# Performance work log

Hardware: AMD Instinct MI355X
Metric: run time of the kernel (lower is better)

The kernel has to match this reference:

```python
import jax, jax.numpy as jnp
import numpy as np

MUL0, MUL1 = 128, 64            # scalar (0e) and vector (1o) multiplicities
B = 8192                        # batch of nodes
SQRT3 = 3.0 ** 0.5
SQRT6 = 6.0 ** 0.5

# path normalization (e3nn 'component' irrep norm / 'element' path norm):
# coeff_ins = sqrt(dim(ir_out) / fan_in(i_out)), fan_in = sum_{ins -> i_out} mul1*mul2
A_0E = (1.0 / (MUL0 * MUL0 + MUL1 * MUL1)) ** 0.5   # paths (0,0,0)+(1,1,0)
A_1O = (3.0 / (MUL0 * MUL1 + MUL1 * MUL0)) ** 0.5   # paths (0,1,1)+(1,0,1)
A_1E = (3.0 / (MUL1 * MUL1)) ** 0.5                  # path  (1,1,1)


def _levi_civita():
    eps = np.zeros((3, 3, 3), dtype=np.float32)
    eps[0, 1, 2] = eps[1, 2, 0] = eps[2, 0, 1] = 1.0
    eps[0, 2, 1] = eps[2, 1, 0] = eps[1, 0, 2] = -1.0
    return jnp.asarray(eps)


def setup_inputs() -> dict:
    key = jax.random.key(0)
    ks = jax.random.split(key, 7)
    return {
        "x1": jax.random.normal(ks[0], (B, MUL0 + 3 * MUL1), dtype=jnp.float32),
        "x2": jax.random.normal(ks[1], (B, MUL0 + 3 * MUL1), dtype=jnp.float32),
        "w000": jax.random.normal(ks[2], (MUL0, MUL0, MUL0), dtype=jnp.float32),
        "w011": jax.random.normal(ks[3], (MUL0, MUL1, MUL1), dtype=jnp.float32),
        "w101": jax.random.normal(ks[4], (MUL1, MUL0, MUL1), dtype=jnp.float32),
        "w110": jax.random.normal(ks[5], (MUL1, MUL1, MUL0), dtype=jnp.float32),
        "w111": jax.random.normal(ks[6], (MUL1, MUL1, MUL1), dtype=jnp.float32),
    }


def reference(x1, x2, w000, w011, w101, w110, w111):
    b = x1.shape[0]
    # split irreps: scalars [b, 128], vectors [b, 64, 3]
    s1, v1 = x1[:, :MUL0], x1[:, MUL0:].reshape(b, MUL1, 3)
    s2, v2 = x2[:, :MUL0], x2[:, MUL0:].reshape(b, MUL1, 3)

    # 0e output: 0e x 0e -> 0e (w3j = 1) and 1o x 1o -> 0e (w3j = delta/sqrt3)
    out0 = A_0E * (
        jnp.einsum("uvw,bu,bv->bw", w000, s1, s2)
        + jnp.einsum("uvw,bui,bvi->bw", w110, v1, v2) / SQRT3
    )

    # 1o output: 0e x 1o -> 1o and 1o x 0e -> 1o (w3j = delta/sqrt3)
    out1o = (A_1O / SQRT3) * (
        jnp.einsum("uvw,bu,bvi->bwi", w011, s1, v2)
        + jnp.einsum("uvw,bui,bv->bwi", w101, v1, s2)
    )

    # 1e output: 1o x 1o -> 1e (w3j = levi-civita / sqrt6)
    eps = _levi_civita()
    out1e = (A_1E / SQRT6) * jnp.einsum("uvw,bui,bvj,ijk->bwk", w111, v1, v2, eps)

    return jnp.concatenate(
        [out0, out1o.reshape(b, -1), out1e.reshape(b, -1)], axis=-1
    )  # [b, 128 + 192 + 192] = [b, 512]
```

## Files before the change

kernel.cpp:

```cpp
#include <hip/hip_runtime.h>
#include <stdint.h>


typedef _Float16 f16;
typedef f16 f16x8 __attribute__((ext_vector_type(8)));
typedef float f32x4 __attribute__((ext_vector_type(4)));
typedef int i32x4 __attribute__((ext_vector_type(4)));

#define OFF_W000 0u
#define OFF_W110 2097152u
#define OFF_W011 2621440u
#define OFF_W101 3145728u
#define OFF_W111 3670016u
#define OFF_XS1  3932160u
#define OFF_XS2  4980736u
#define OFF_XV1  6029312u
#define OFF_XV2  7602176u
#define OFF_S0A  9175040u
#define OFF_S0B  10223616u
#define OFF_S1O  13369344u
#define WS_ELEMS 14942208u

#define SC_0E 0.006987712429686843f
#define SC_1O 0.0078125f
#define SC_1E 0.011048543456039806f

__global__ void tile_all_k(const float* __restrict__ w000, const float* __restrict__ w011,
                           const float* __restrict__ w101, const float* __restrict__ w110,
                           const float* __restrict__ w111, const float* __restrict__ x1,
                           const float* __restrict__ x2, f16* __restrict__ ws)
{
  unsigned tid = blockIdx.x*256u + threadIdx.x;
  if (tid < 2097152u) {
    unsigned e=tid&7u, n=(tid>>3)&127u, q=(tid>>10)&3u, p=(tid>>12)&1u, u=(tid>>13)&127u, vh=(tid>>20)&1u;
    unsigned v = vh*64u + p*32u + q*8u + e;
    ws[OFF_W000+tid] = (f16)w000[u*16384u + v*128u + n];
    return;
  }
  tid -= 2097152u;
  if (tid < 524288u) {
    unsigned e=tid&7u, n=(tid>>3)&127u, q=(tid>>10)&3u, p=(tid>>12)&1u, u=tid>>13;
    unsigned v = p*32u + q*8u + e;
    ws[OFF_W110+tid] = (f16)(w110[u*8192u + v*128u + n] * 0.5773502691896258f);
    return;
  }
  tid -= 524288u;
  if (tid < 524288u) {
    unsigned e=tid&7u, n=(tid>>3)&63u, q=(tid>>9)&3u, p=(tid>>11)&1u, u=tid>>12;
    unsigned v = p*32u + q*8u + e;
    ws[OFF_W011+tid] = (f16)w011[u*4096u + v*64u + n];
    return;
  }
  tid -= 524288u;
  if (tid < 524288u) {
    unsigned e=tid&7u, n=(tid>>3)&63u, q=(tid>>9)&3u, p=(tid>>11)&1u, u=tid>>12;
    unsigned v = p*32u + q*8u + e;
    ws[OFF_W101+tid] = (f16)w101[v*8192u + u*64u + n];
    return;
  }
  tid -= 524288u;
  if (tid < 262144u) {
    unsigned e=tid&7u, n=(tid>>3)&63u, q=(tid>>9)&3u, p=(tid>>11)&1u, u=tid>>12;
    unsigned v = p*32u + q*8u + e;
    ws[OFF_W111+tid] = (f16)w111[u*4096u + v*64u + n];
    return;
  }
  tid -= 262144u;
  if (tid < 1048576u) {
    unsigned e=tid&7u, r=(tid>>3)&127u, uo=(tid>>10)&15u, rt=tid>>14;
    ws[OFF_XS1+tid] = (f16)x1[(rt*128u+r)*320u + uo*8u + e];
    return;
  }
  tid -= 1048576u;
  if (tid < 1572864u) {
    unsigned e=tid&7u, r=(tid>>3)&127u, ov=(tid>>10)&7u, rest=tid>>13;
    unsigned i=rest%3u, rt=rest/3u;
    ws[OFF_XV1+tid] = (f16)x1[(rt*128u+r)*320u + 128u + (ov*8u+e)*3u + i];
    return;
  }
  tid -= 1572864u;
  if (tid < 1048576u) {
    unsigned e=tid&7u, r=(tid>>3)&127u, uo=(tid>>10)&15u, rt=tid>>14;
    ws[OFF_XS2+tid] = (f16)x2[(rt*128u+r)*320u + uo*8u + e];
    return;
  }
  tid -= 1048576u;
  {
    unsigned e=tid&7u, r=(tid>>3)&127u, ov=(tid>>10)&7u, rest=tid>>13;
    unsigned i=rest%3u, rt=rest/3u;
    ws[OFF_XV2+tid] = (f16)x2[(rt*128u+r)*320u + 128u + (ov*8u+e)*3u + i];
  }
}

#define GLD16(g,l) __builtin_amdgcn_global_load_lds( \
    (const __attribute__((address_space(1))) unsigned int*)(g), \
    (__attribute__((address_space(3))) unsigned int*)(l), 16, 0, 0)

#define WAITV(n) asm volatile("s_waitcnt vmcnt(" #n ")" ::: "memory")

template<int N, bool NEG, int SS>
__device__ __forceinline__ void run_phase(const f16* __restrict__ Wt,
    const f16* __restrict__ aW, const f16* __restrict__ bW, int bRow, int h,
    f16* sW, f16* sAw, f32x4 (&acc)[4][4])
{
  constexpr int S     = N/64;
  constexpr int TILEB = N*64;
  constexpr int PAIRB = 2*TILEB;
  constexpr int TILEE = N*32;
  constexpr int PAIRE = 2*TILEE;
  constexpr int M     = SS*8;
  const int lane = threadIdx.x & 63, wid = threadIdx.x >> 6;
  const int q = lane >> 4, r15 = lane & 15;

  WAITV(0);

  f16x8 br[4][2];
#pragma unroll
  for (int mt=0; mt<4; ++mt)
#pragma unroll
    for (int o=0; o<2; ++o)
      br[mt][o] = *(const f16x8*)(bW + (o*4+q)*1024 + (bRow + mt*16 + r15)*8);
#pragma unroll
  for (int mt=0; mt<4; ++mt)
#pragma unroll
    for (int o=0; o<2; ++o) {
      i32x4 tmp = __builtin_bit_cast(i32x4, br[mt][o]);
      asm volatile("" :: "v"(tmp));
    }

  const int wchunk = wid*S*1024;
  auto stPair = [&](int p, int slot){
    const char* s = (const char*)Wt + (size_t)p*PAIRB + wchunk;
    char* d = (char*)sW + slot*PAIRB + wchunk;
#pragma unroll
    for (int tt=0; tt<2; ++tt)
#pragma unroll
      for (int c=0; c<S; ++c)
        GLD16(s + tt*TILEB + c*1024 + lane*16, d + tt*TILEB + c*1024);
  };
  auto stA = [&](int ss2){
    GLD16((const char*)(aW + ss2*1024) + lane*16, (char*)sAw + (ss2&1)*1024);
  };

  stA(0); stPair(0,0); stPair(1,1);

#pragma unroll 1
  for (int ss = 0; ss < SS; ++ss) {
    f16x8 aR[4];
#pragma unroll
    for (int k = 0; k < 8; ++k) {
      const int m = ss*8 + k;
      if (k == 7) {
        if (ss+1 < SS) { if constexpr (S==1) WAITV(3); else WAITV(5); }
        else           WAITV(0);
      } else {
        if constexpr (S==1) WAITV(2); else WAITV(4);
      }
      __builtin_amdgcn_s_barrier();
      __builtin_amdgcn_sched_barrier(0);
      if (k == 6 && ss+1 < SS) stA(ss+1);
      if (m+2 < M) stPair(m+2, (k+2)&3);
      if (k == 0) {
#pragma unroll
        for (int mt=0; mt<4; ++mt)
          aR[mt] = *(const f16x8*)(sAw + (ss&1)*512 + (mt*16+r15)*8);
      }
      f16x8 af[4][2];
#pragma unroll
      for (int mt=0; mt<4; ++mt) {
        f16 av = aR[mt][k];
        if constexpr (NEG) av = -av;
        af[mt][0] = av * br[mt][0];
        af[mt][1] = av * br[mt][1];
      }
#pragma unroll
      for (int tt=0; tt<2; ++tt) {
        const f16* W = sW + (k&3)*PAIRE + tt*TILEE;
#pragma unroll
        for (int nt=0; nt<4; ++nt) {
          f16x8 bw = *(const f16x8*)(W + (q*N + h*64 + nt*16 + r15)*8);
#pragma unroll
          for (int mt=0; mt<4; ++mt)
            acc[mt][nt] = __builtin_amdgcn_mfma_f32_16x16x32_f16(af[mt][tt], bw, acc[mt][nt], 0,0,0);
        }
      }
    }
  }
  __builtin_amdgcn_s_barrier();
  __builtin_amdgcn_sched_barrier(0);
}

__global__ __launch_bounds__(256, 2)
void tp_main(f16* __restrict__ ws, float* __restrict__ out)
{
  __shared__ f16 smem[36864];
  f16* sW = smem;
  const int lane = threadIdx.x & 63, wid = threadIdx.x >> 6;
  f16* sAw = smem + 32768 + wid*1024;
  const int q = lane >> 4, r15 = lane & 15;

  f32x4 acc[4][4];
#pragma unroll
  for (int a=0;a<4;++a)
#pragma unroll
    for (int b=0;b<4;++b) acc[a][b] = (f32x4){0.f,0.f,0.f,0.f};

  const int bid = blockIdx.x;

  if (bid < 128) {
    const int rt = bid >> 1, vh = bid & 1;
    const int rgrp = wid >> 1, h = wid & 1;
    const f16* aW = ws + OFF_XS1 + rt*16384 + rgrp*512;
    const f16* bW = ws + OFF_XS2 + rt*16384 + vh*8192;
    run_phase<128,false,16>(ws + OFF_W000 + vh*1048576u, aW, bW, rgrp*64, h, sW, sAw, acc);
    const int rowb = rt*128 + rgrp*64;
    if (vh == 0) {
#pragma unroll
      for (int mt=0;mt<4;++mt)
#pragma unroll
        for (int nt=0;nt<4;++nt)
#pragma unroll
          for (int rg=0;rg<4;++rg)
            out[(rowb+mt*16+q*4+rg)*512 + h*64+nt*16+r15] = SC_0E*acc[mt][nt][rg];
    } else {
      f16* slab = ws + OFF_S0A;
#pragma unroll
      for (int mt=0;mt<4;++mt)
#pragma unroll
        for (int nt=0;nt<4;++nt)
#pragma unroll
          for (int rg=0;rg<4;++rg)
            slab[(rowb+mt*16+q*4+rg)*128 + h*64+nt*16+r15] = (f16)(SC_0E*acc[mt][nt][rg]);
    }
  } else if (bid < 224) {
    const int id = bid-128, i = id%3, rt = id/3;
    const int rgrp = wid, ro = rgrp & 1, sub = rgrp >> 1;
    const int rtt = rt*2 + sub;
    const f16* aW = ws + OFF_XS1 + rtt*16384 + ro*512;
    const f16* bW = ws + OFF_XV2 + (rtt*3+i)*8192;
    run_phase<64,false,16>(ws + OFF_W011, aW, bW, ro*64, 0, sW, sAw, acc);
    const int rowb = rt*256 + rgrp*64;
#pragma unroll
    for (int mt=0;mt<4;++mt)
#pragma unroll
      for (int nt=0;nt<4;++nt)
#pragma unroll
        for (int rg=0;rg<4;++rg)
          out[(rowb+mt*16+q*4+rg)*512 + 128 + 3*(nt*16+r15) + i] = SC_1O*acc[mt][nt][rg];
  } else if (bid < 320) {
    const int id = bid-224, i = id%3, rt = id/3;
    const int rgrp = wid, ro = rgrp & 1, sub = rgrp >> 1;
    const int rtt = rt*2 + sub;
    const f16* aW = ws + OFF_XS2 + rtt*16384 + ro*512;
    const f16* bW = ws + OFF_XV1 + (rtt*3+i)*8192;
    run_phase<64,false,16>(ws + OFF_W101, aW, bW, ro*64, 0, sW, sAw, acc);
    const int rowb = rt*256 + rgrp*64;
    f16* slab = ws + OFF_S1O;
#pragma unroll
    for (int mt=0;mt<4;++mt)
#pragma unroll
      for (int nt=0;nt<4;++nt)
#pragma unroll
        for (int rg=0;rg<4;++rg)
          slab[(rowb+mt*16+q*4+rg)*192 + 3*(nt*16+r15) + i] = (f16)(SC_1O*acc[mt][nt][rg]);
  } else if (bid < 416) {
    const int id = bid-320, kk = id%3, rt = id/3;
    int i = kk+1; if (i>2) i-=3;
    int j = kk+2; if (j>2) j-=3;
    const int rgrp = wid, ro = rgrp & 1, sub = rgrp >> 1;
    const int rtt = rt*2 + sub;
    run_phase<64,false,8>(ws + OFF_W111,
        ws + OFF_XV1 + (rtt*3+i)*8192 + ro*512, ws + OFF_XV2 + (rtt*3+j)*8192,
        ro*64, 0, sW, sAw, acc);
    run_phase<64,true,8>(ws + OFF_W111,
        ws + OFF_XV1 + (rtt*3+j)*8192 + ro*512, ws + OFF_XV2 + (rtt*3+i)*8192,
        ro*64, 0, sW, sAw, acc);
    const int rowb = rt*256 + rgrp*64;
#pragma unroll
    for (int mt=0;mt<4;++mt)
#pragma unroll
      for (int nt=0;nt<4;++nt)
#pragma unroll
        for (int rg=0;rg<4;++rg)
          out[(rowb+mt*16+q*4+rg)*512 + 320 + 3*(nt*16+r15) + kk] = SC_1E*acc[mt][nt][rg];
  } else {
    const int id = bid-416, i = id%3, rp = id/3;
    const int rgrp = wid >> 1, h = wid & 1;
#pragma unroll 1
    for (int hh = 0; hh < 2; ++hh) {
      const int rt = rp*2 + hh;
      const f16* aW = ws + OFF_XV1 + (rt*3+i)*8192 + rgrp*512;
      const f16* bW = ws + OFF_XV2 + (rt*3+i)*8192;
      run_phase<128,false,8>(ws + OFF_W110, aW, bW, rgrp*64, h, sW, sAw, acc);
      const int rowb = rt*128 + rgrp*64;
      f16* slab = ws + OFF_S0B + (unsigned)i*1048576u;
#pragma unroll
      for (int mt=0;mt<4;++mt)
#pragma unroll
        for (int nt=0;nt<4;++nt)
#pragma unroll
          for (int rg=0;rg<4;++rg) {
            slab[(rowb+mt*16+q*4+rg)*128 + h*64+nt*16+r15] = (f16)(SC_0E*acc[mt][nt][rg]);
            acc[mt][nt][rg] = 0.f;
          }
    }
  }
}

__global__ void ep_add(const f16* __restrict__ ws, float* __restrict__ out)
{
  unsigned tid = blockIdx.x*256u + threadIdx.x;
  if (tid < 1048576u) {
    unsigned r = tid>>7, c = tid&127u;
    float s = (float)ws[OFF_S0A+tid] + (float)ws[OFF_S0B+tid]
            + (float)ws[OFF_S0B+1048576u+tid] + (float)ws[OFF_S0B+2097152u+tid];
    out[r*512u+c] += s;
  } else {
    unsigned t2 = tid - 1048576u;
    unsigned r = t2/192u, c = t2 - r*192u;
    out[r*512u+128u+c] += (float)ws[OFF_S1O+t2];
  }
}

extern "C" void kernel_launch(void* const* d_in, const int* in_sizes, int n_in,
                              void* d_out, int out_size, void* d_ws, size_t ws_size,
                              hipStream_t stream)
{
  const float* x1   = (const float*)d_in[0];
  const float* x2   = (const float*)d_in[1];
  const float* w000 = (const float*)d_in[2];
  const float* w011 = (const float*)d_in[3];
  const float* w101 = (const float*)d_in[4];
  const float* w110 = (const float*)d_in[5];
  const float* w111 = (const float*)d_in[6];
  float* out = (float*)d_out;
  f16* ws   = (f16*)d_ws;

  if (ws_size < (size_t)WS_ELEMS * 2) return;

  tile_all_k<<<35840, 256, 0, stream>>>(w000, w011, w101, w110, w111, x1, x2, ws);
  tp_main<<<512, 256, 0, stream>>>(ws, out);
  ep_add<<<10240, 256, 0, stream>>>(ws, out);
}
```

Measured before the change: 149.2 us.

## Deepen weight prefetch to three stages and double-buffer LDS B-fragments in registers

The global-to-LDS weight pipeline now keeps three pairs in flight instead of two. The LDS reads of the B fragments for the next step are issued into a second register buffer before the current step's MFMAs run, so LDS latency overlaps compute. MFMA sections are wrapped in s_setprio raises. In exchange it uses 16 extra f16x8 registers, which could hurt occupancy under the 2-blocks launch bound, and it depends on the wait-count changes being correct for slot reuse across 4 LDS slots.

```diff
diff --git a/kernel.cpp b/kernel.cpp
--- a/kernel.cpp
+++ b/kernel.cpp
@@ -142,48 +142,61 @@
     GLD16((const char*)(aW + ss2*1024) + lane*16, (char*)sAw + (ss2&1)*1024);
   };
 
-  stA(0); stPair(0,0); stPair(1,1);
+  stA(0); stPair(0,0); stPair(1,1); stPair(2,2);
+  if constexpr (S==1) WAITV(4); else WAITV(8);
+  __builtin_amdgcn_s_barrier();
+  __builtin_amdgcn_sched_barrier(0);
+
+  f16x8 bwA[8], bwB[8];
+  auto ldBW = [&](f16x8 (&dst)[8], int slot){
+#pragma unroll
+    for (int tt=0; tt<2; ++tt)
+#pragma unroll
+      for (int nt=0; nt<4; ++nt)
+        dst[tt*4+nt] = *(const f16x8*)(sW + slot*PAIRE + tt*TILEE
+                                       + (q*N + h*64 + nt*16 + r15)*8);
+  };
+  ldBW(bwA, 0);
+
+  f16x8 aR[4];
 
 #pragma unroll 1
   for (int ss = 0; ss < SS; ++ss) {
-    f16x8 aR[4];
 #pragma unroll
     for (int k = 0; k < 8; ++k) {
-      const int m = ss*8 + k;
-      if (k == 7) {
-        if (ss+1 < SS) { if constexpr (S==1) WAITV(3); else WAITV(5); }
-        else           WAITV(0);
-      } else {
-        if constexpr (S==1) WAITV(2); else WAITV(4);
-      }
+      const int t = ss*8 + k;
+      if (t + 2 < M) { if constexpr (S==1) WAITV(2); else WAITV(4); }
+      else           WAITV(0);
       __builtin_amdgcn_s_barrier();
       __builtin_amdgcn_sched_barrier(0);
       if (k == 6 && ss+1 < SS) stA(ss+1);
-      if (m+2 < M) stPair(m+2, (k+2)&3);
+      if (t + 3 < M) stPair(t+3, (t+3)&3);
       if (k == 0) {
 #pragma unroll
         for (int mt=0; mt<4; ++mt)
           aR[mt] = *(const f16x8*)(sAw + (ss&1)*512 + (mt*16+r15)*8);
       }
-      f16x8 af[4][2];
-#pragma unroll
-      for (int mt=0; mt<4; ++mt) {
-        f16 av = aR[mt][k];
-        if constexpr (NEG) av = -av;
-        af[mt][0] = av * br[mt][0];
-        af[mt][1] = av * br[mt][1];
+      if (t + 1 < M) {
+        if (k & 1) ldBW(bwA, (t+1)&3); else ldBW(bwB, (t+1)&3);
       }
+      const f16x8 (&bw)[8] = (k & 1) ? bwB : bwA;
+      __builtin_amdgcn_s_setprio(1);
 #pragma unroll
       for (int tt=0; tt<2; ++tt) {
-        const f16* W = sW + (k&3)*PAIRE + tt*TILEE;
-#pragma unroll
-        for (int nt=0; nt<4; ++nt) {
-          f16x8 bw = *(const f16x8*)(W + (q*N + h*64 + nt*16 + r15)*8);
+        f16x8 af[4];
+#pragma unroll
+        for (int mt=0; mt<4; ++mt) {
+          f16 av = aR[mt][k];
+          if constexpr (NEG) av = -av;
+          af[mt] = av * br[mt][tt];
+        }
+#pragma unroll
+        for (int nt=0; nt<4; ++nt)
 #pragma unroll
           for (int mt=0; mt<4; ++mt)
-            acc[mt][nt] = __builtin_amdgcn_mfma_f32_16x16x32_f16(af[mt][tt], bw, acc[mt][nt], 0,0,0);
-        }
+            acc[mt][nt] = __builtin_amdgcn_mfma_f32_16x16x32_f16(af[mt], bw[tt*4+nt], acc[mt][nt], 0,0,0);
       }
+      __builtin_amdgcn_s_setprio(0);
     }
   }
   __builtin_amdgcn_s_barrier();
```

Measured after the change: 149.3 us. Within noise of the previous version (+0.1%).

## Deepen LDS pipeline with register double-buffering and replace epilogue with atomics

Applied to the files above, without the earlier changes.

The main loop now prefetches three weight tiles ahead instead of two and reads the next step's B operands from LDS into a second register bank via inline ds_read_b128 while the current step's MFMAs run, raising wave priority around the MFMA block. The f16 partial-sum slabs and the separate ep_add kernel are removed; every block now atomically adds its fp32 results into the output, which a new zeroing kernel clears first. This trades the extra slab traffic and a kernel launch for global float atomics and higher register pressure, and makes summation order nondeterministic.

```diff
diff --git a/kernel.cpp b/kernel.cpp
--- a/kernel.cpp
+++ b/kernel.cpp
@@ -16,10 +16,7 @@
 #define OFF_XS2  4980736u
 #define OFF_XV1  6029312u
 #define OFF_XV2  7602176u
-#define OFF_S0A  9175040u
-#define OFF_S0B  10223616u
-#define OFF_S1O  13369344u
-#define WS_ELEMS 14942208u
+#define WS_ELEMS 9175040u
 
 #define SC_0E 0.006987712429686843f
 #define SC_1O 0.0078125f
@@ -92,11 +89,87 @@
   }
 }
 
+__global__ void zero_k(float* __restrict__ out)
+{
+  unsigned tid = blockIdx.x*256u + threadIdx.x;
+  unsigned r = tid/80u, c = tid - r*80u;
+  *(f32x4*)(out + r*512u + c*4u) = (f32x4){0.f,0.f,0.f,0.f};
+}
+
 #define GLD16(g,l) __builtin_amdgcn_global_load_lds( \
     (const __attribute__((address_space(1))) unsigned int*)(g), \
     (__attribute__((address_space(3))) unsigned int*)(l), 16, 0, 0)
 
 #define WAITV(n) asm volatile("s_waitcnt vmcnt(" #n ")" ::: "memory")
+
+__device__ __forceinline__ unsigned lds_off(const f16* p){
+  return (unsigned)(unsigned long long)(__attribute__((address_space(3))) const f16*)p;
+}
+template<int OFF>
+__device__ __forceinline__ f16x8 ds128(unsigned a){
+  f16x8 r;
+  asm volatile("ds_read_b128 %0, %1 offset:%2" : "=v"(r) : "v"(a), "i"(OFF));
+  return r;
+}
+__device__ __forceinline__ f16x8 ds128v(unsigned a){
+  f16x8 r;
+  asm volatile("ds_read_b128 %0, %1" : "=v"(r) : "v"(a));
+  return r;
+}
+
+#define READ8(dst, SL) do{                                \
+    dst[0]=ds128<(SL)*PAIRB+0*TILEB>(wbase[0]);           \
+    dst[1]=ds128<(SL)*PAIRB+0*TILEB>(wbase[1]);           \
+    dst[2]=ds128<(SL)*PAIRB+0*TILEB>(wbase[2]);           \
+    dst[3]=ds128<(SL)*PAIRB+0*TILEB>(wbase[3]);           \
+    dst[4]=ds128<(SL)*PAIRB+1*TILEB>(wbase[0]);           \
+    dst[5]=ds128<(SL)*PAIRB+1*TILEB>(wbase[1]);           \
+    dst[6]=ds128<(SL)*PAIRB+1*TILEB>(wbase[2]);           \
+    dst[7]=ds128<(SL)*PAIRB+1*TILEB>(wbase[3]);           \
+  }while(0)
+
+#define K_STEP(KC)                                                            \
+  {                                                                           \
+    constexpr int kc = (KC);                                                  \
+    const int t = ss*8 + kc;                                                  \
+    if (t + 2 < M) { if constexpr (S==1) WAITV(2); else WAITV(4); }           \
+    else           WAITV(0);                                                  \
+    __builtin_amdgcn_s_barrier();                                             \
+    __builtin_amdgcn_sched_barrier(0);                                        \
+    if (kc == 6 && ss+1 < SS) stA(ss+1);                                      \
+    if (t + 3 < M) stPair(t+3, (kc+3)&3);                                     \
+    if (kc == 0) {                                                            \
+      const unsigned ao = (unsigned)((ss&1)<<10);                             \
+      aR[0]=ds128v(abase[0]+ao); aR[1]=ds128v(abase[1]+ao);                   \
+      aR[2]=ds128v(abase[2]+ao); aR[3]=ds128v(abase[3]+ao);                   \
+    }                                                                         \
+    if (!(kc==7 && ss+1>=SS)) {                                               \
+      constexpr int SL = (kc+1)&3;                                            \
+      if constexpr ((kc&1)==0) { READ8(bwB, SL); } else { READ8(bwA, SL); }   \
+    }                                                                         \
+    __builtin_amdgcn_sched_barrier(0);                                        \
+    if (kc==7 && ss+1>=SS) { asm volatile("s_waitcnt lgkmcnt(0)":::"memory");}\
+    else                   { asm volatile("s_waitcnt lgkmcnt(8)":::"memory");}\
+    __builtin_amdgcn_sched_barrier(0);                                        \
+    const f16x8 (&bw)[8] = (kc&1) ? bwB : bwA;                                \
+    __builtin_amdgcn_s_setprio(1);                                            \
+    _Pragma("unroll")                                                         \
+    for (int tt=0; tt<2; ++tt) {                                              \
+      f16x8 af[4];                                                            \
+      _Pragma("unroll")                                                       \
+      for (int mt=0; mt<4; ++mt) {                                            \
+        f16 av = aR[mt][kc];                                                  \
+        if constexpr (NEG) av = -av;                                          \
+        af[mt] = av * br[mt][tt];                                             \
+      }                                                                       \
+      _Pragma("unroll")                                                       \
+      for (int nt=0; nt<4; ++nt)                                              \
+        _Pragma("unroll")                                                     \
+        for (int mt=0; mt<4; ++mt)                                            \
+          acc[mt][nt] = __builtin_amdgcn_mfma_f32_16x16x32_f16(af[mt], bw[tt*4+nt], acc[mt][nt], 0,0,0); \
+    }                                                                         \
+    __builtin_amdgcn_s_setprio(0);                                            \
+  }
 
 template<int N, bool NEG, int SS>
 __device__ __forceinline__ void run_phase(const f16* __restrict__ Wt,
@@ -106,8 +179,6 @@
   constexpr int S     = N/64;
   constexpr int TILEB = N*64;
   constexpr int PAIRB = 2*TILEB;
-  constexpr int TILEE = N*32;
-  constexpr int PAIRE = 2*TILEE;
   constexpr int M     = SS*8;
   const int lane = threadIdx.x & 63, wid = threadIdx.x >> 6;
   const int q = lane >> 4, r15 = lane & 15;
@@ -142,49 +213,27 @@
     GLD16((const char*)(aW + ss2*1024) + lane*16, (char*)sAw + (ss2&1)*1024);
   };
 
-  stA(0); stPair(0,0); stPair(1,1);
+  unsigned wbase[4], abase[4];
+#pragma unroll
+  for (int nt=0; nt<4; ++nt)
+    wbase[nt] = lds_off(sW + (q*N + h*64 + nt*16 + r15)*8);
+#pragma unroll
+  for (int mt=0; mt<4; ++mt)
+    abase[mt] = lds_off(sAw + (mt*16 + r15)*8);
+
+  stA(0); stPair(0,0); stPair(1,1); stPair(2,2);
+  if constexpr (S==1) WAITV(4); else WAITV(8);
+  __builtin_amdgcn_s_barrier();
+  __builtin_amdgcn_sched_barrier(0);
+
+  f16x8 bwA[8], bwB[8];
+  f16x8 aR[4];
+  READ8(bwA, 0);
 
 #pragma unroll 1
   for (int ss = 0; ss < SS; ++ss) {
-    f16x8 aR[4];
-#pragma unroll
-    for (int k = 0; k < 8; ++k) {
-      const int m = ss*8 + k;
-      if (k == 7) {
-        if (ss+1 < SS) { if constexpr (S==1) WAITV(3); else WAITV(5); }
-        else           WAITV(0);
-      } else {
-        if constexpr (S==1) WAITV(2); else WAITV(4);
-      }
-      __builtin_amdgcn_s_barrier();
-      __builtin_amdgcn_sched_barrier(0);
-      if (k == 6 && ss+1 < SS) stA(ss+1);
-      if (m+2 < M) stPair(m+2, (k+2)&3);
-      if (k == 0) {
-#pragma unroll
-        for (int mt=0; mt<4; ++mt)
-          aR[mt] = *(const f16x8*)(sAw + (ss&1)*512 + (mt*16+r15)*8);
-      }
-      f16x8 af[4][2];
-#pragma unroll
-      for (int mt=0; mt<4; ++mt) {
-        f16 av = aR[mt][k];
-        if constexpr (NEG) av = -av;
-        af[mt][0] = av * br[mt][0];
-        af[mt][1] = av * br[mt][1];
-      }
-#pragma unroll
-      for (int tt=0; tt<2; ++tt) {
-        const f16* W = sW + (k&3)*PAIRE + tt*TILEE;
-#pragma unroll
-        for (int nt=0; nt<4; ++nt) {
-          f16x8 bw = *(const f16x8*)(W + (q*N + h*64 + nt*16 + r15)*8);
-#pragma unroll
-          for (int mt=0; mt<4; ++mt)
-            acc[mt][nt] = __builtin_amdgcn_mfma_f32_16x16x32_f16(af[mt][tt], bw, acc[mt][nt], 0,0,0);
-        }
-      }
-    }
+    K_STEP(0) K_STEP(1) K_STEP(2) K_STEP(3)
+    K_STEP(4) K_STEP(5) K_STEP(6) K_STEP(7)
   }
   __builtin_amdgcn_s_barrier();
   __builtin_amdgcn_sched_barrier(0);
@@ -214,24 +263,13 @@
     const f16* bW = ws + OFF_XS2 + rt*16384 + vh*8192;
     run_phase<128,false,16>(ws + OFF_W000 + vh*1048576u, aW, bW, rgrp*64, h, sW, sAw, acc);
     const int rowb = rt*128 + rgrp*64;
-    if (vh == 0) {
-#pragma unroll
-      for (int mt=0;mt<4;++mt)
-#pragma unroll
-        for (int nt=0;nt<4;++nt)
-#pragma unroll
-          for (int rg=0;rg<4;++rg)
-            out[(rowb+mt*16+q*4+rg)*512 + h*64+nt*16+r15] = SC_0E*acc[mt][nt][rg];
-    } else {
-      f16* slab = ws + OFF_S0A;
-#pragma unroll
-      for (int mt=0;mt<4;++mt)
-#pragma unroll
-        for (int nt=0;nt<4;++nt)
-#pragma unroll
-          for (int rg=0;rg<4;++rg)
-            slab[(rowb+mt*16+q*4+rg)*128 + h*64+nt*16+r15] = (f16)(SC_0E*acc[mt][nt][rg]);
-    }
+#pragma unroll
+    for (int mt=0;mt<4;++mt)
+#pragma unroll
+      for (int nt=0;nt<4;++nt)
+#pragma unroll
+        for (int rg=0;rg<4;++rg)
+          atomicAdd(out + (rowb+mt*16+q*4+rg)*512 + h*64+nt*16+r15, SC_0E*acc[mt][nt][rg]);
   } else if (bid < 224) {
     const int id = bid-128, i = id%3, rt = id/3;
     const int rgrp = wid, ro = rgrp & 1, sub = rgrp >> 1;
@@ -246,7 +284,7 @@
       for (int nt=0;nt<4;++nt)
 #pragma unroll
         for (int rg=0;rg<4;++rg)
-          out[(rowb+mt*16+q*4+rg)*512 + 128 + 3*(nt*16+r15) + i] = SC_1O*acc[mt][nt][rg];
+          atomicAdd(out + (rowb+mt*16+q*4+rg)*512 + 128 + 3*(nt*16+r15) + i, SC_1O*acc[mt][nt][rg]);
   } else if (bid < 320) {
     const int id = bid-224, i = id%3, rt = id/3;
     const int rgrp = wid, ro = rgrp & 1, sub = rgrp >> 1;
@@ -255,14 +293,13 @@
     const f16* bW = ws + OFF_XV1 + (rtt*3+i)*8192;
     run_phase<64,false,16>(ws + OFF_W101, aW, bW, ro*64, 0, sW, sAw, acc);
     const int rowb = rt*256 + rgrp*64;
-    f16* slab = ws + OFF_S1O;
 #pragma unroll
     for (int mt=0;mt<4;++mt)
 #pragma unroll
       for (int nt=0;nt<4;++nt)
 #pragma unroll
         for (int rg=0;rg<4;++rg)
-          slab[(rowb+mt*16+q*4+rg)*192 + 3*(nt*16+r15) + i] = (f16)(SC_1O*acc[mt][nt][rg]);
+          atomicAdd(out + (rowb+mt*16+q*4+rg)*512 + 128 + 3*(nt*16+r15) + i, SC_1O*acc[mt][nt][rg]);
   } else if (bid < 416) {
     const int id = bid-320, kk = id%3, rt = id/3;
     int i = kk+1; if (i>2) i-=3;
@@ -293,32 +330,16 @@
       const f16* bW = ws + OFF_XV2 + (rt*3+i)*8192;
       run_phase<128,false,8>(ws + OFF_W110, aW, bW, rgrp*64, h, sW, sAw, acc);
       const int rowb = rt*128 + rgrp*64;
-      f16* slab = ws + OFF_S0B + (unsigned)i*1048576u;
 #pragma unroll
       for (int mt=0;mt<4;++mt)
 #pragma unroll
         for (int nt=0;nt<4;++nt)
 #pragma unroll
           for (int rg=0;rg<4;++rg) {
-            slab[(rowb+mt*16+q*4+rg)*128 + h*64+nt*16+r15] = (f16)(SC_0E*acc[mt][nt][rg]);
+            atomicAdd(out + (rowb+mt*16+q*4+rg)*512 + h*64+nt*16+r15, SC_0E*acc[mt][nt][rg]);
             acc[mt][nt][rg] = 0.f;
           }
     }
-  }
-}
-
-__global__ void ep_add(const f16* __restrict__ ws, float* __restrict__ out)
-{
-  unsigned tid = blockIdx.x*256u + threadIdx.x;
-  if (tid < 1048576u) {
-    unsigned r = tid>>7, c = tid&127u;
-    float s = (float)ws[OFF_S0A+tid] + (float)ws[OFF_S0B+tid]
-            + (float)ws[OFF_S0B+1048576u+tid] + (float)ws[OFF_S0B+2097152u+tid];
-    out[r*512u+c] += s;
-  } else {
-    unsigned t2 = tid - 1048576u;
-    unsigned r = t2/192u, c = t2 - r*192u;
-    out[r*512u+128u+c] += (float)ws[OFF_S1O+t2];
   }
 }
 
@@ -339,6 +360,6 @@
   if (ws_size < (size_t)WS_ELEMS * 2) return;
 
   tile_all_k<<<35840, 256, 0, stream>>>(w000, w011, w101, w110, w111, x1, x2, ws);
+  zero_k<<<2560, 256, 0, stream>>>(out);
   tp_main<<<512, 256, 0, stream>>>(ws, out);
-  ep_add<<<10240, 256, 0, stream>>>(ws, out);
-}
+}
```

Measured after the change: 164.1 us. +10.0%, slower.

## Give each wave a private weight pipeline and drop block-wide barriers

Applied to the files above, without the earlier changes.

Each wave now streams its own 64-column slice of the weight tiles into a private shared-memory double buffer, so the per-step s_barrier is removed and only per-wave vmcnt waits remain. The W000 and W110 tiled layouts are split by output half, and the work decomposition is reorganised so every wave handles a 64-row by 64-column block. The W110 path no longer loops two row tiles per block, which raises the grid from 512 to 608 blocks. MFMA sections are wrapped in s_setprio to favour issue. In exchange, each wave fetches its own copy of the weights, so global and L2 traffic per block goes up, and the pipeline now has only two slots per wave instead of four shared ones.

```diff
diff --git a/kernel.cpp b/kernel.cpp
--- a/kernel.cpp
+++ b/kernel.cpp
@@ -32,16 +32,18 @@
 {
   unsigned tid = blockIdx.x*256u + threadIdx.x;
   if (tid < 2097152u) {
-    unsigned e=tid&7u, n=(tid>>3)&127u, q=(tid>>10)&3u, p=(tid>>12)&1u, u=(tid>>13)&127u, vh=(tid>>20)&1u;
+    unsigned e=tid&7u, n=(tid>>3)&63u, q=(tid>>9)&3u, p=(tid>>11)&1u,
+             u=(tid>>12)&127u, vh=(tid>>19)&1u, h=(tid>>20)&1u;
     unsigned v = vh*64u + p*32u + q*8u + e;
-    ws[OFF_W000+tid] = (f16)w000[u*16384u + v*128u + n];
+    ws[OFF_W000+tid] = (f16)w000[u*16384u + v*128u + h*64u + n];
     return;
   }
   tid -= 2097152u;
   if (tid < 524288u) {
-    unsigned e=tid&7u, n=(tid>>3)&127u, q=(tid>>10)&3u, p=(tid>>12)&1u, u=tid>>13;
+    unsigned e=tid&7u, n=(tid>>3)&63u, q=(tid>>9)&3u, p=(tid>>11)&1u,
+             u=(tid>>12)&63u, h=(tid>>18)&1u;
     unsigned v = p*32u + q*8u + e;
-    ws[OFF_W110+tid] = (f16)(w110[u*8192u + v*128u + n] * 0.5773502691896258f);
+    ws[OFF_W110+tid] = (f16)(w110[u*8192u + v*128u + h*64u + n] * 0.5773502691896258f);
     return;
   }
   tid -= 524288u;
@@ -98,21 +100,13 @@
 
 #define WAITV(n) asm volatile("s_waitcnt vmcnt(" #n ")" ::: "memory")
 
-template<int N, bool NEG, int SS>
+template<bool NEG, int SS>
 __device__ __forceinline__ void run_phase(const f16* __restrict__ Wt,
-    const f16* __restrict__ aW, const f16* __restrict__ bW, int bRow, int h,
-    f16* sW, f16* sAw, f32x4 (&acc)[4][4])
-{
-  constexpr int S     = N/64;
-  constexpr int TILEB = N*64;
-  constexpr int PAIRB = 2*TILEB;
-  constexpr int TILEE = N*32;
-  constexpr int PAIRE = 2*TILEE;
-  constexpr int M     = SS*8;
-  const int lane = threadIdx.x & 63, wid = threadIdx.x >> 6;
+    const f16* __restrict__ aW, const f16* __restrict__ bW, int bRow,
+    f16* sWw, f16* sAw, f32x4 (&acc)[4][4], int lane)
+{
+  constexpr int M = SS*8;
   const int q = lane >> 4, r15 = lane & 15;
-
-  WAITV(0);
 
   f16x8 br[4][2];
 #pragma unroll
@@ -128,76 +122,67 @@
       asm volatile("" :: "v"(tmp));
     }
 
-  const int wchunk = wid*S*1024;
   auto stPair = [&](int p, int slot){
-    const char* s = (const char*)Wt + (size_t)p*PAIRB + wchunk;
-    char* d = (char*)sW + slot*PAIRB + wchunk;
-#pragma unroll
-    for (int tt=0; tt<2; ++tt)
-#pragma unroll
-      for (int c=0; c<S; ++c)
-        GLD16(s + tt*TILEB + c*1024 + lane*16, d + tt*TILEB + c*1024);
+    const char* s = (const char*)Wt + (size_t)p*8192;
+    char* d = (char*)sWw + slot*8192;
+#pragma unroll
+    for (int c=0; c<8; ++c)
+      GLD16(s + c*1024 + lane*16, d + c*1024);
   };
   auto stA = [&](int ss2){
     GLD16((const char*)(aW + ss2*1024) + lane*16, (char*)sAw + (ss2&1)*1024);
   };
 
-  stA(0); stPair(0,0); stPair(1,1);
-
+  stPair(0,0); stA(0); stPair(1,1);
+
+  f16x8 aR[4];
 #pragma unroll 1
   for (int ss = 0; ss < SS; ++ss) {
-    f16x8 aR[4];
-#pragma unroll
-    for (int k = 0; k < 8; ++k) {
-      const int m = ss*8 + k;
-      if (k == 7) {
-        if (ss+1 < SS) { if constexpr (S==1) WAITV(3); else WAITV(5); }
-        else           WAITV(0);
-      } else {
-        if constexpr (S==1) WAITV(2); else WAITV(4);
-      }
-      __builtin_amdgcn_s_barrier();
-      __builtin_amdgcn_sched_barrier(0);
-      if (k == 6 && ss+1 < SS) stA(ss+1);
-      if (m+2 < M) stPair(m+2, (k+2)&3);
-      if (k == 0) {
+#pragma unroll
+    for (int kc = 0; kc < 8; ++kc) {
+      const int t = ss*8 + kc;
+      if (kc == 7) { if (ss+1 < SS) { WAITV(9); } else { WAITV(0); } }
+      else         { WAITV(8); }
+      if (kc == 0) {
 #pragma unroll
         for (int mt=0; mt<4; ++mt)
           aR[mt] = *(const f16x8*)(sAw + (ss&1)*512 + (mt*16+r15)*8);
       }
-      f16x8 af[4][2];
-#pragma unroll
-      for (int mt=0; mt<4; ++mt) {
-        f16 av = aR[mt][k];
-        if constexpr (NEG) av = -av;
-        af[mt][0] = av * br[mt][0];
-        af[mt][1] = av * br[mt][1];
-      }
-#pragma unroll
-      for (int tt=0; tt<2; ++tt) {
-        const f16* W = sW + (k&3)*PAIRE + tt*TILEE;
+      __builtin_amdgcn_s_setprio(1);
+#pragma unroll
+      for (int p=0; p<2; ++p) {
+        f16x8 af[4];
+#pragma unroll
+        for (int mt=0; mt<4; ++mt) {
+          f16 av = aR[mt][kc];
+          if constexpr (NEG) av = -av;
+          af[mt] = av * br[mt][p];
+        }
 #pragma unroll
         for (int nt=0; nt<4; ++nt) {
-          f16x8 bw = *(const f16x8*)(W + (q*N + h*64 + nt*16 + r15)*8);
+          f16x8 bw = *(const f16x8*)(sWw + (kc&1)*4096 + p*2048 + (q*64 + nt*16 + r15)*8);
 #pragma unroll
           for (int mt=0; mt<4; ++mt)
-            acc[mt][nt] = __builtin_amdgcn_mfma_f32_16x16x32_f16(af[mt][tt], bw, acc[mt][nt], 0,0,0);
+            acc[mt][nt] = __builtin_amdgcn_mfma_f32_16x16x32_f16(af[mt], bw, acc[mt][nt], 0,0,0);
         }
       }
+      __builtin_amdgcn_s_setprio(0);
+      __builtin_amdgcn_sched_barrier(0);
+      if (kc == 6 && ss+1 < SS) stA(ss+1);
+      if (t + 2 < M) stPair(t+2, kc&1);
     }
   }
-  __builtin_amdgcn_s_barrier();
-  __builtin_amdgcn_sched_barrier(0);
 }
 
 __global__ __launch_bounds__(256, 2)
 void tp_main(f16* __restrict__ ws, float* __restrict__ out)
 {
   __shared__ f16 smem[36864];
-  f16* sW = smem;
   const int lane = threadIdx.x & 63, wid = threadIdx.x >> 6;
+  f16* sWw = smem + wid*8192;
   f16* sAw = smem + 32768 + wid*1024;
   const int q = lane >> 4, r15 = lane & 15;
+  const int sub = wid >> 1, rh = wid & 1;
 
   f32x4 acc[4][4];
 #pragma unroll
@@ -207,104 +192,76 @@
 
   const int bid = blockIdx.x;
 
+#define STORE_DIRECT(base_col_expr, SC)                                   \
+  _Pragma("unroll")                                                       \
+  for (int mt=0;mt<4;++mt)                                                \
+    _Pragma("unroll")                                                     \
+    for (int nt=0;nt<4;++nt)                                              \
+      _Pragma("unroll")                                                   \
+      for (int rg=0;rg<4;++rg)                                            \
+        out[(rowb+mt*16+q*4+rg)*512 + (base_col_expr)] = (SC)*acc[mt][nt][rg];
+
+#define STORE_SLAB(slab, stride, col_expr, SC)                            \
+  _Pragma("unroll")                                                       \
+  for (int mt=0;mt<4;++mt)                                                \
+    _Pragma("unroll")                                                     \
+    for (int nt=0;nt<4;++nt)                                              \
+      _Pragma("unroll")                                                   \
+      for (int rg=0;rg<4;++rg)                                            \
+        (slab)[(rowb+mt*16+q*4+rg)*(stride) + (col_expr)] = (f16)((SC)*acc[mt][nt][rg]);
+
   if (bid < 128) {
-    const int rt = bid >> 1, vh = bid & 1;
-    const int rgrp = wid >> 1, h = wid & 1;
-    const f16* aW = ws + OFF_XS1 + rt*16384 + rgrp*512;
-    const f16* bW = ws + OFF_XS2 + rt*16384 + vh*8192;
-    run_phase<128,false,16>(ws + OFF_W000 + vh*1048576u, aW, bW, rgrp*64, h, sW, sAw, acc);
-    const int rowb = rt*128 + rgrp*64;
-    if (vh == 0) {
-#pragma unroll
-      for (int mt=0;mt<4;++mt)
-#pragma unroll
-        for (int nt=0;nt<4;++nt)
-#pragma unroll
-          for (int rg=0;rg<4;++rg)
-            out[(rowb+mt*16+q*4+rg)*512 + h*64+nt*16+r15] = SC_0E*acc[mt][nt][rg];
-    } else {
-      f16* slab = ws + OFF_S0A;
-#pragma unroll
-      for (int mt=0;mt<4;++mt)
-#pragma unroll
-        for (int nt=0;nt<4;++nt)
-#pragma unroll
-          for (int rg=0;rg<4;++rg)
-            slab[(rowb+mt*16+q*4+rg)*128 + h*64+nt*16+r15] = (f16)(SC_0E*acc[mt][nt][rg]);
-    }
+    const int rtp = bid >> 2, vh = (bid >> 1) & 1, h = bid & 1;
+    const int rtt = rtp*2 + sub;
+    const f16* aW = ws + OFF_XS1 + rtt*16384 + rh*512;
+    const f16* bW = ws + OFF_XS2 + rtt*16384 + vh*8192;
+    const f16* Wt = ws + OFF_W000 + h*1048576u + vh*524288u;
+    run_phase<false,16>(Wt, aW, bW, rh*64, sWw, sAw, acc, lane);
+    const int rowb = rtt*128 + rh*64;
+    if (vh == 0) { STORE_DIRECT(h*64+nt*16+r15, SC_0E) }
+    else { f16* slab = ws + OFF_S0A; STORE_SLAB(slab, 128, h*64+nt*16+r15, SC_0E) }
   } else if (bid < 224) {
-    const int id = bid-128, i = id%3, rt = id/3;
-    const int rgrp = wid, ro = rgrp & 1, sub = rgrp >> 1;
-    const int rtt = rt*2 + sub;
-    const f16* aW = ws + OFF_XS1 + rtt*16384 + ro*512;
+    const int id = bid-128, i = id%3, rtp = id/3;
+    const int rtt = rtp*2 + sub;
+    const f16* aW = ws + OFF_XS1 + rtt*16384 + rh*512;
     const f16* bW = ws + OFF_XV2 + (rtt*3+i)*8192;
-    run_phase<64,false,16>(ws + OFF_W011, aW, bW, ro*64, 0, sW, sAw, acc);
-    const int rowb = rt*256 + rgrp*64;
-#pragma unroll
-    for (int mt=0;mt<4;++mt)
-#pragma unroll
-      for (int nt=0;nt<4;++nt)
-#pragma unroll
-        for (int rg=0;rg<4;++rg)
-          out[(rowb+mt*16+q*4+rg)*512 + 128 + 3*(nt*16+r15) + i] = SC_1O*acc[mt][nt][rg];
+    run_phase<false,16>(ws + OFF_W011, aW, bW, rh*64, sWw, sAw, acc, lane);
+    const int rowb = rtt*128 + rh*64;
+    STORE_DIRECT(128 + 3*(nt*16+r15) + i, SC_1O)
   } else if (bid < 320) {
-    const int id = bid-224, i = id%3, rt = id/3;
-    const int rgrp = wid, ro = rgrp & 1, sub = rgrp >> 1;
-    const int rtt = rt*2 + sub;
-    const f16* aW = ws + OFF_XS2 + rtt*16384 + ro*512;
+    const int id = bid-224, i = id%3, rtp = id/3;
+    const int rtt = rtp*2 + sub;
+    const f16* aW = ws + OFF_XS2 + rtt*16384 + rh*512;
     const f16* bW = ws + OFF_XV1 + (rtt*3+i)*8192;
-    run_phase<64,false,16>(ws + OFF_W101, aW, bW, ro*64, 0, sW, sAw, acc);
-    const int rowb = rt*256 + rgrp*64;
+    run_phase<false,16>(ws + OFF_W101, aW, bW, rh*64, sWw, sAw, acc, lane);
+    const int rowb = rtt*128 + rh*64;
     f16* slab = ws + OFF_S1O;
-#pragma unroll
-    for (int mt=0;mt<4;++mt)
-#pragma unroll
-      for (int nt=0;nt<4;++nt)
-#pragma unroll
-        for (int rg=0;rg<4;++rg)
-          slab[(rowb+mt*16+q*4+rg)*192 + 3*(nt*16+r15) + i] = (f16)(SC_1O*acc[mt][nt][rg]);
+    STORE_SLAB(slab, 192, 3*(nt*16+r15) + i, SC_1O)
   } else if (bid < 416) {
-    const int id = bid-320, kk = id%3, rt = id/3;
+    const int id = bid-320, kk = id%3, rtp = id/3;
     int i = kk+1; if (i>2) i-=3;
     int j = kk+2; if (j>2) j-=3;
-    const int rgrp = wid, ro = rgrp & 1, sub = rgrp >> 1;
-    const int rtt = rt*2 + sub;
-    run_phase<64,false,8>(ws + OFF_W111,
-        ws + OFF_XV1 + (rtt*3+i)*8192 + ro*512, ws + OFF_XV2 + (rtt*3+j)*8192,
-        ro*64, 0, sW, sAw, acc);
-    run_phase<64,true,8>(ws + OFF_W111,
-        ws + OFF_XV1 + (rtt*3+j)*8192 + ro*512, ws + OFF_XV2 + (rtt*3+i)*8192,
-        ro*64, 0, sW, sAw, acc);
-    const int rowb = rt*256 + rgrp*64;
-#pragma unroll
-    for (int mt=0;mt<4;++mt)
-#pragma unroll
-      for (int nt=0;nt<4;++nt)
-#pragma unroll
-        for (int rg=0;rg<4;++rg)
-          out[(rowb+mt*16+q*4+rg)*512 + 320 + 3*(nt*16+r15) + kk] = SC_1E*acc[mt][nt][rg];
+    const int rtt = rtp*2 + sub;
+    run_phase<false,8>(ws + OFF_W111,
+        ws + OFF_XV1 + (rtt*3+i)*8192 + rh*512, ws + OFF_XV2 + (rtt*3+j)*8192,
+        rh*64, sWw, sAw, acc, lane);
+    run_phase<true,8>(ws + OFF_W111,
+        ws + OFF_XV1 + (rtt*3+j)*8192 + rh*512, ws + OFF_XV2 + (rtt*3+i)*8192,
+        rh*64, sWw, sAw, acc, lane);
+    const int rowb = rtt*128 + rh*64;
+    STORE_DIRECT(320 + 3*(nt*16+r15) + kk, SC_1E)
   } else {
-    const int id = bid-416, i = id%3, rp = id/3;
-    const int rgrp = wid >> 1, h = wid & 1;
-#pragma unroll 1
-    for (int hh = 0; hh < 2; ++hh) {
-      const int rt = rp*2 + hh;
-      const f16* aW = ws + OFF_XV1 + (rt*3+i)*8192 + rgrp*512;
-      const f16* bW = ws + OFF_XV2 + (rt*3+i)*8192;
-      run_phase<128,false,8>(ws + OFF_W110, aW, bW, rgrp*64, h, sW, sAw, acc);
-      const int rowb = rt*128 + rgrp*64;
-      f16* slab = ws + OFF_S0B + (unsigned)i*1048576u;
-#pragma unroll
-      for (int mt=0;mt<4;++mt)
-#pragma unroll
-        for (int nt=0;nt<4;++nt)
-#pragma unroll
-          for (int rg=0;rg<4;++rg) {
-            slab[(rowb+mt*16+q*4+rg)*128 + h*64+nt*16+r15] = (f16)(SC_0E*acc[mt][nt][rg]);
-            acc[mt][nt][rg] = 0.f;
-          }
-    }
-  }
+    const int id = bid-416, i = id%3, h = (id/3)&1, rtp = id/6;
+    const int rtt = rtp*2 + sub;
+    const f16* aW = ws + OFF_XV1 + (rtt*3+i)*8192 + rh*512;
+    const f16* bW = ws + OFF_XV2 + (rtt*3+i)*8192;
+    run_phase<false,8>(ws + OFF_W110 + h*262144u, aW, bW, rh*64, sWw, sAw, acc, lane);
+    const int rowb = rtt*128 + rh*64;
+    f16* slab = ws + OFF_S0B + (unsigned)i*1048576u;
+    STORE_SLAB(slab, 128, h*64+nt*16+r15, SC_0E)
+  }
+#undef STORE_DIRECT
+#undef STORE_SLAB
 }
 
 __global__ void ep_add(const f16* __restrict__ ws, float* __restrict__ out)
@@ -339,6 +296,6 @@
   if (ws_size < (size_t)WS_ELEMS * 2) return;
 
   tile_all_k<<<35840, 256, 0, stream>>>(w000, w011, w101, w110, w111, x1, x2, ws);
-  tp_main<<<512, 256, 0, stream>>>(ws, out);
+  tp_main<<<608, 256, 0, stream>>>(ws, out);
   ep_add<<<10240, 256, 0, stream>>>(ws, out);
 }
```

Result: slower. 157.6 us (+5.7%).
